# Kernel optimization log

Hardware: AMD Instinct MI355X
Metric: run time of the kernel (lower is better)

Reference implementation:

```python
import jax, jax.numpy as jnp
import numpy as np

B, H, W, C = 8, 128, 128, 384
WS, SHIFT, NH = 8, 4, 12
N = WS * WS            # tokens per window = 64
HD = C // NH           # head dim = 32
SCALE = HD ** -0.5


def _rel_pos_index():
    ch, cw = np.meshgrid(np.arange(WS), np.arange(WS), indexing='ij')
    cf = np.stack([ch.ravel(), cw.ravel()])            # (2, N)
    rel = cf[:, :, None] - cf[:, None, :]              # (2, N, N)
    rel = rel.transpose(1, 2, 0)                       # (N, N, 2)
    rel[:, :, 0] += WS - 1
    rel[:, :, 1] += WS - 1
    rel[:, :, 0] *= 2 * WS - 1
    return jnp.asarray(rel.sum(-1))                    # (N, N) int

REL_IDX = _rel_pos_index()


def _shift_mask():
    # standard Swin SW-MSA mask, built once with numpy
    img = np.zeros((1, H, W, 1), np.float32)
    cnt = 0
    for hs in (slice(0, -WS), slice(-WS, -SHIFT), slice(-SHIFT, None)):
        for ws_ in (slice(0, -WS), slice(-WS, -SHIFT), slice(-SHIFT, None)):
            img[:, hs, ws_, :] = cnt
            cnt += 1
    m = img.reshape(1, H // WS, WS, W // WS, WS, 1).transpose(0, 1, 3, 2, 4, 5)
    m = m.reshape(-1, N)                               # (nW, N)
    am = m[:, None, :] - m[:, :, None]                 # (nW, N, N)
    return np.where(am != 0, np.float32(-100.0), np.float32(0.0))


def _ln(x, g, b, eps=1e-5):
    mu = x.mean(-1, keepdims=True)
    var = ((x - mu) ** 2).mean(-1, keepdims=True)
    return (x - mu) * jax.lax.rsqrt(var + eps) * g + b


def setup_inputs() -> dict:
    key = jax.random.key(0)
    ks = jax.random.split(key, 10)
    s = 0.02
    return {
        'x': jax.random.normal(ks[0], (B, H * W, C), jnp.float32),
        'qkv_w': jax.random.normal(ks[1], (3 * C, C), jnp.float32) * s,
        'qkv_b': jnp.zeros((3 * C,), jnp.float32),
        'proj_w': jax.random.normal(ks[2], (C, C), jnp.float32) * s,
        'proj_b': jnp.zeros((C,), jnp.float32),
        'rel_bias_table': jax.random.normal(ks[3], ((2 * WS - 1) ** 2, NH), jnp.float32) * s,
        'g1': jnp.ones((C,), jnp.float32), 'b1': jnp.zeros((C,), jnp.float32),
        'g2': jnp.ones((C,), jnp.float32), 'b2': jnp.zeros((C,), jnp.float32),
        'fc1_w': jax.random.normal(ks[4], (4 * C, C), jnp.float32) * s,
        'fc1_b': jnp.zeros((4 * C,), jnp.float32),
        'fc2_w': jax.random.normal(ks[5], (C, 4 * C), jnp.float32) * s,
        'fc2_b': jnp.zeros((C,), jnp.float32),
        'attn_mask': jnp.asarray(_shift_mask()),       # (nW, N, N)
    }


def reference(x, qkv_w, qkv_b, proj_w, proj_b, rel_bias_table, g1, b1, g2, b2,
              fc1_w, fc1_b, fc2_w, fc2_b, attn_mask):
    shortcut = x
    h = _ln(x, g1, b1).reshape(B, H, W, C)
    # cyclic shift (SW-MSA)
    h = jnp.roll(h, (-SHIFT, -SHIFT), axis=(1, 2))
    # window partition -> (B*nW, N, C)
    nWh, nWw = H // WS, W // WS
    hw = h.reshape(B, nWh, WS, nWw, WS, C).transpose(0, 1, 3, 2, 4, 5)
    hw = hw.reshape(B * nWh * nWw, N, C)
    # qkv projection
    qkv = jnp.einsum('bnc,dc->bnd', hw, qkv_w) + qkv_b   # (Bw, N, 3C)
    qkv = qkv.reshape(-1, N, 3, NH, HD).transpose(2, 0, 3, 1, 4)
    q, k, v = qkv[0], qkv[1], qkv[2]                    # (Bw, NH, N, HD)
    attn = jnp.einsum('bhnd,bhmd->bhnm', q * SCALE, k)  # (Bw, NH, N, N)
    bias = rel_bias_table[REL_IDX.reshape(-1)].reshape(N, N, NH)
    attn = attn + bias.transpose(2, 0, 1)[None]
    # shift mask: attn viewed as (B, nW, NH, N, N) + mask (nW, 1, N, N)
    nW = nWh * nWw
    attn = attn.reshape(B, nW, NH, N, N) + attn_mask[None, :, None]
    attn = jax.nn.softmax(attn.reshape(-1, NH, N, N), axis=-1)
    out = jnp.einsum('bhnm,bhmd->bnhd', attn, v).reshape(-1, N, C)
    out = jnp.einsum('bnc,dc->bnd', out, proj_w) + proj_b
    # window reverse + un-shift
    out = out.reshape(B, nWh, nWw, WS, WS, C).transpose(0, 1, 3, 2, 4, 5)
    out = out.reshape(B, H, W, C)
    out = jnp.roll(out, (SHIFT, SHIFT), axis=(1, 2)).reshape(B, H * W, C)
    x = shortcut + out
    # MLP block
    h2 = _ln(x, g2, b2)
    h2 = jax.nn.gelu(jnp.einsum('blc,dc->bld', h2, fc1_w) + fc1_b, approximate=False)
    h2 = jnp.einsum('bld,cd->blc', h2, fc2_w) + fc2_b
    return x + h2
```

## Files before the change

kernel.cpp:

```cpp
#include <hip/hip_runtime.h>
#include <hip/hip_bf16.h>
#include <math.h>

typedef __attribute__((ext_vector_type(4))) float f32x4;
typedef __attribute__((ext_vector_type(8))) short bf16x8;

__device__ __forceinline__ unsigned short f2bf(float f) {
  unsigned int x = __builtin_bit_cast(unsigned int, f);
  x += 0x7fffu + ((x >> 16) & 1u);
  return (unsigned short)(x >> 16);
}
__device__ __forceinline__ float bf2f(unsigned short u) {
  unsigned int x = ((unsigned int)u) << 16;
  return __builtin_bit_cast(float, x);
}

__device__ __forceinline__ void gload_lds16(const void* g, void* l) {
  __builtin_amdgcn_global_load_lds(
      (const __attribute__((address_space(1))) unsigned int*)g,
      (__attribute__((address_space(3))) unsigned int*)l, 16, 0, 0);
}

__global__ void cvt_f32_bf16(const float* __restrict__ s, unsigned short* __restrict__ d, int n) {
  int i = blockIdx.x * 256 + threadIdx.x;
  if (i < n) d[i] = f2bf(s[i]);
}

template <int REMAP>
__global__ __launch_bounds__(256)
void ln_kernel(const float* __restrict__ x, const float* __restrict__ g,
               const float* __restrict__ b, unsigned short* __restrict__ dst_o) {
  int r = blockIdx.x * 4 + (threadIdx.x >> 6);
  int lane = threadIdx.x & 63;
  size_t src;
  if (REMAP) {
    int w = r >> 6, t = r & 63;
    int bb = w >> 8, wi = (w >> 4) & 15, wj = w & 15;
    int i = t >> 3, j = t & 7;
    int p = (wi * 8 + i + 4) & 127, q = (wj * 8 + j + 4) & 127;
    src = ((size_t)bb * 16384 + p * 128 + q) * 384;
  } else {
    src = (size_t)r * 384;
  }
  float v[6];
  float s = 0.f, s2 = 0.f;
#pragma unroll
  for (int m = 0; m < 6; ++m) {
    v[m] = x[src + lane + 64 * m];
    s += v[m];
    s2 += v[m] * v[m];
  }
#pragma unroll
  for (int o2 = 1; o2 < 64; o2 <<= 1) {
    s += __shfl_xor(s, o2);
    s2 += __shfl_xor(s2, o2);
  }
  float mu = s * (1.f / 384.f);
  float var = s2 * (1.f / 384.f) - mu * mu;
  float ri = rsqrtf(var + 1e-5f);
  size_t dst = (size_t)r * 384;
#pragma unroll
  for (int m = 0; m < 6; ++m) {
    int c = lane + 64 * m;
    dst_o[dst + c] = f2bf((v[m] - mu) * ri * g[c] + b[c]);
  }
}

__global__ __launch_bounds__(256)
void ln_bf16(const unsigned short* __restrict__ x, const float* __restrict__ g,
             const float* __restrict__ b, unsigned short* __restrict__ dst_o) {
  int r = blockIdx.x * 4 + (threadIdx.x >> 6);
  int lane = threadIdx.x & 63;
  size_t src = (size_t)r * 384;
  float v[6];
  float s = 0.f, s2 = 0.f;
#pragma unroll
  for (int m = 0; m < 3; ++m) {
    unsigned int u = *(const unsigned int*)&x[src + lane * 2 + 128 * m];
    v[2 * m] = bf2f((unsigned short)(u & 0xffffu));
    v[2 * m + 1] = bf2f((unsigned short)(u >> 16));
    s += v[2 * m] + v[2 * m + 1];
    s2 += v[2 * m] * v[2 * m] + v[2 * m + 1] * v[2 * m + 1];
  }
#pragma unroll
  for (int o2 = 1; o2 < 64; o2 <<= 1) {
    s += __shfl_xor(s, o2);
    s2 += __shfl_xor(s2, o2);
  }
  float mu = s * (1.f / 384.f);
  float var = s2 * (1.f / 384.f) - mu * mu;
  float ri = rsqrtf(var + 1e-5f);
#pragma unroll
  for (int m = 0; m < 3; ++m) {
    int c = lane * 2 + 128 * m;
    unsigned int lo = f2bf((v[2 * m] - mu) * ri * g[c] + b[c]);
    unsigned int hi = f2bf((v[2 * m + 1] - mu) * ri * g[c + 1] + b[c + 1]);
    *(unsigned int*)&dst_o[src + c] = lo | (hi << 16);
  }
}

template <int EPI>
__global__ __launch_bounds__(256, 2)
void gemm_bt(const unsigned short* __restrict__ A, const unsigned short* __restrict__ Bw,
             const float* __restrict__ bias, int M, int N, int K, int NT,
             unsigned short* __restrict__ Obf, const void* __restrict__ resid,
             float* __restrict__ Of) {
  __shared__ unsigned short smA[2][128 * 64];
  __shared__ unsigned short smB[2][128 * 64];
  const int tid = threadIdx.x;
  const int lane = tid & 63;
  const int wid = tid >> 6;
  const int wm = wid >> 1, wn = wid & 1;
  const int li = lane & 15, lg = lane >> 4;

  const int nwg = gridDim.x;
  const int orig = blockIdx.x;
  const int q = nwg >> 3, r = nwg & 7;
  const int xcd = orig & 7, loc = orig >> 3;
  const int wg = (xcd < r ? xcd * (q + 1) : r * (q + 1) + (xcd - r) * q) + loc;
  const int m0 = (wg / NT) * 128;
  const int n0 = (wg % NT) * 128;

  const int srow = wid * 8 + (lane >> 3);
  const int scol = ((lane & 7) ^ (lane >> 3)) * 8;
  const unsigned short* gA = A + (size_t)(m0 + srow) * K + scol;
  const unsigned short* gB = Bw + (size_t)(n0 + srow) * K + scol;

  f32x4 acc[4][4] = {};
  const int nk = K >> 6;
  const int fswz = (li & 7) << 3;

#pragma unroll
  for (int c = 0; c < 4; ++c) {
    gload_lds16(gA + (size_t)(c * 32) * K, &smA[0][(c * 32 + wid * 8) * 64]);
    gload_lds16(gB + (size_t)(c * 32) * K, &smB[0][(c * 32 + wid * 8) * 64]);
  }
  __syncthreads();

  for (int k0 = 0; k0 < nk; ++k0) {
    const int cur = k0 & 1;
    if (k0 + 1 < nk) {
#pragma unroll
      for (int c = 0; c < 4; ++c) {
        gload_lds16(gA + (size_t)(c * 32) * K + (k0 + 1) * 64,
                    &smA[cur ^ 1][(c * 32 + wid * 8) * 64]);
        gload_lds16(gB + (size_t)(c * 32) * K + (k0 + 1) * 64,
                    &smB[cur ^ 1][(c * 32 + wid * 8) * 64]);
      }
    }
#pragma unroll
    for (int kk = 0; kk < 2; ++kk) {
      bf16x8 a[4], bb[4];
#pragma unroll
      for (int f = 0; f < 4; ++f) {
        a[f] = *(const bf16x8*)&smA[cur][(wm * 64 + f * 16 + li) * 64 + ((kk * 32 + lg * 8) ^ fswz)];
        bb[f] = *(const bf16x8*)&smB[cur][(wn * 64 + f * 16 + li) * 64 + ((kk * 32 + lg * 8) ^ fswz)];
      }
#pragma unroll
      for (int mf = 0; mf < 4; ++mf)
#pragma unroll
        for (int nf = 0; nf < 4; ++nf)
          acc[mf][nf] = __builtin_amdgcn_mfma_f32_16x16x32_bf16(a[mf], bb[nf], acc[mf][nf], 0, 0, 0);
    }
    __syncthreads();
  }

#pragma unroll
  for (int mf = 0; mf < 4; ++mf) {
#pragma unroll
    for (int r2 = 0; r2 < 4; ++r2) {
      int mrow = m0 + wm * 64 + mf * 16 + lg * 4 + r2;
      size_t orow = (size_t)mrow;
      if (EPI == 2) {
        int w = mrow >> 6, t = mrow & 63;
        int bb2 = w >> 8, wi = (w >> 4) & 15, wj = w & 15;
        int i = t >> 3, j = t & 7;
        int p = (wi * 8 + i + 4) & 127, qq = (wj * 8 + j + 4) & 127;
        orow = (size_t)bb2 * 16384 + p * 128 + qq;
      }
#pragma unroll
      for (int nf = 0; nf < 4; ++nf) {
        int col = n0 + wn * 64 + nf * 16 + li;
        float v = acc[mf][nf][r2] + bias[col];
        if (EPI == 0) {
          Obf[(size_t)mrow * N + col] = f2bf(v);
        } else if (EPI == 1) {
          float y = 1.5957691f * (v + 0.044715f * v * v * v);
          float gl = v * __builtin_amdgcn_rcpf(1.f + __expf(-y));
          Obf[(size_t)mrow * N + col] = f2bf(gl);
        } else if (EPI == 2) {
          const float* rx = (const float*)resid;
          Obf[orow * 384 + col] = f2bf(v + rx[orow * 384 + col]);
        } else {
          const unsigned short* rx = (const unsigned short*)resid;
          Of[(size_t)mrow * N + col] = v + bf2f(rx[(size_t)mrow * N + col]);
        }
      }
    }
  }
}

__global__ __launch_bounds__(256, 2)
void attn_kernel(const unsigned short* __restrict__ qkv, const float* __restrict__ btab,
                 const float* __restrict__ mask, unsigned short* __restrict__ out) {
  __shared__ unsigned short v_lds[4][64 * 40];
  __shared__ unsigned short p_lds[4][64 * 72];
  const int w = blockIdx.x;
  const int tid = threadIdx.x;
  const int wid = tid >> 6, lane = tid & 63;
  const int li = lane & 15, lg = lane >> 4;
  const float* mrow = mask + (size_t)(w & 255) * 4096;
  const size_t base = (size_t)w * 64;
  const float SC = 0.17677669529663688f;

#pragma unroll 1
  for (int hi = 0; hi < 3; ++hi) {
    int h = wid * 3 + hi;
    bf16x8 aq[4], bk[4];
#pragma unroll
    for (int f = 0; f < 4; ++f) {
      size_t off = (base + f * 16 + li) * 1152 + h * 32 + lg * 8;
      aq[f] = *(const bf16x8*)&qkv[off];
      bk[f] = *(const bf16x8*)&qkv[off + 384];
    }
    f32x4 s[4][4] = {};
#pragma unroll
    for (int mf = 0; mf < 4; ++mf)
#pragma unroll
      for (int nf = 0; nf < 4; ++nf)
        s[mf][nf] = __builtin_amdgcn_mfma_f32_16x16x32_bf16(aq[mf], bk[nf], s[mf][nf], 0, 0, 0);

    {
      const unsigned short* vp = &qkv[(base + lane) * 1152 + 768 + h * 32];
      unsigned short* dp = &v_lds[wid][lane * 40];
#pragma unroll
      for (int c = 0; c < 4; ++c) *(bf16x8*)&dp[c * 8] = *(const bf16x8*)&vp[c * 8];
    }

#pragma unroll
    for (int mf = 0; mf < 4; ++mf) {
#pragma unroll
      for (int r = 0; r < 4; ++r) {
        int m = mf * 16 + lg * 4 + r;
        float mx = -1e30f;
#pragma unroll
        for (int nf = 0; nf < 4; ++nf) {
          int n = nf * 16 + li;
          int ridx = ((m >> 3) - (n >> 3) + 7) * 15 + (m & 7) - (n & 7) + 7;
          float val = s[mf][nf][r] * SC + btab[ridx * 12 + h] + mrow[m * 64 + n];
          s[mf][nf][r] = val;
          mx = fmaxf(mx, val);
        }
#pragma unroll
        for (int o2 = 1; o2 < 16; o2 <<= 1) mx = fmaxf(mx, __shfl_xor(mx, o2));
        float sum = 0.f;
#pragma unroll
        for (int nf = 0; nf < 4; ++nf) {
          float e = __expf(s[mf][nf][r] - mx);
          s[mf][nf][r] = e;
          sum += e;
        }
#pragma unroll
        for (int o2 = 1; o2 < 16; o2 <<= 1) sum += __shfl_xor(sum, o2);
        float inv = __builtin_amdgcn_rcpf(sum);
#pragma unroll
        for (int nf = 0; nf < 4; ++nf) s[mf][nf][r] *= inv;
      }
    }

#pragma unroll
    for (int mf = 0; mf < 4; ++mf)
#pragma unroll
      for (int nf = 0; nf < 4; ++nf)
#pragma unroll
        for (int r = 0; r < 4; ++r) {
          int m = mf * 16 + lg * 4 + r, n = nf * 16 + li;
          p_lds[wid][m * 72 + n] = f2bf(s[mf][nf][r]);
        }

    f32x4 o[4][2] = {};
#pragma unroll
    for (int kf = 0; kf < 2; ++kf) {
      bf16x8 bv[2];
#pragma unroll
      for (int df = 0; df < 2; ++df) {
        bf16x8 t;
#pragma unroll
        for (int e = 0; e < 8; ++e)
          t[e] = (short)v_lds[wid][(kf * 32 + lg * 8 + e) * 40 + df * 16 + li];
        bv[df] = t;
      }
#pragma unroll
      for (int mf = 0; mf < 4; ++mf) {
        bf16x8 pa = *(const bf16x8*)&p_lds[wid][(mf * 16 + li) * 72 + kf * 32 + lg * 8];
#pragma unroll
        for (int df = 0; df < 2; ++df)
          o[mf][df] = __builtin_amdgcn_mfma_f32_16x16x32_bf16(pa, bv[df], o[mf][df], 0, 0, 0);
      }
    }

#pragma unroll
    for (int mf = 0; mf < 4; ++mf)
#pragma unroll
      for (int df = 0; df < 2; ++df)
#pragma unroll
        for (int r = 0; r < 4; ++r) {
          size_t row = base + mf * 16 + lg * 4 + r;
          out[row * 384 + h * 32 + df * 16 + li] = f2bf(o[mf][df][r]);
        }
  }
}

extern "C" void kernel_launch(void* const* d_in, const int* in_sizes, int n_in,
                              void* d_out, int out_size, void* d_ws, size_t ws_size,
                              hipStream_t stream) {
  const float* x      = (const float*)d_in[0];
  const float* qkv_w  = (const float*)d_in[1];
  const float* qkv_b  = (const float*)d_in[2];
  const float* proj_w = (const float*)d_in[3];
  const float* proj_b = (const float*)d_in[4];
  const float* rel    = (const float*)d_in[5];
  const float* g1     = (const float*)d_in[6];
  const float* b1     = (const float*)d_in[7];
  const float* g2     = (const float*)d_in[8];
  const float* b2     = (const float*)d_in[9];
  const float* fc1_w  = (const float*)d_in[10];
  const float* fc1_b  = (const float*)d_in[11];
  const float* fc2_w  = (const float*)d_in[12];
  const float* fc2_b  = (const float*)d_in[13];
  const float* mask   = (const float*)d_in[14];
  float* out = (float*)d_out;
  char* ws = (char*)d_ws;

  const int M = 131072;
  unsigned short* hw     = (unsigned short*)ws;
  unsigned short* qkv    = (unsigned short*)(ws + 100663296);
  unsigned short* hmid   = (unsigned short*)ws;
  unsigned short* attn_o = (unsigned short*)(ws + 402653184);
  unsigned short* ln2o   = attn_o;
  unsigned short* x1b    = (unsigned short*)(ws + 503316480);
  unsigned short* wq     = (unsigned short*)(ws + 603979776);
  unsigned short* wp     = wq + 442368;
  unsigned short* w1     = wp + 147456;
  unsigned short* w2     = w1 + 589824;

  cvt_f32_bf16<<<(442368 + 255) / 256, 256, 0, stream>>>(qkv_w, wq, 442368);
  cvt_f32_bf16<<<(147456 + 255) / 256, 256, 0, stream>>>(proj_w, wp, 147456);
  cvt_f32_bf16<<<(589824 + 255) / 256, 256, 0, stream>>>(fc1_w, w1, 589824);
  cvt_f32_bf16<<<(589824 + 255) / 256, 256, 0, stream>>>(fc2_w, w2, 589824);

  ln_kernel<1><<<M / 4, 256, 0, stream>>>(x, g1, b1, hw);

  gemm_bt<0><<<9 * 1024, 256, 0, stream>>>(hw, wq, qkv_b, M, 1152, 384, 9, qkv, nullptr, nullptr);

  attn_kernel<<<2048, 256, 0, stream>>>(qkv, rel, mask, attn_o);

  gemm_bt<2><<<3 * 1024, 256, 0, stream>>>(attn_o, wp, proj_b, M, 384, 384, 3, x1b, x, nullptr);

  ln_bf16<<<M / 4, 256, 0, stream>>>(x1b, g2, b2, ln2o);

  gemm_bt<1><<<12 * 1024, 256, 0, stream>>>(ln2o, w1, fc1_b, M, 1536, 384, 12, hmid, nullptr, nullptr);

  gemm_bt<3><<<3 * 1024, 256, 0, stream>>>(hmid, w2, fc2_b, M, 384, 1536, 3, nullptr, x1b, out);
}
```

Measured before the change: 1.178 ms.

## Switch GEMMs to 256x128 tiles with 8 waves and triple-buffered LDS pipeline

Replaces the 128x128, 4-wave, double-buffered GEMM with a 256x128-tile, 512-thread kernel that uses dynamic LDS split into three stages. Loads run two K-steps ahead and are gated by explicit vmcnt waits and a raw s_barrier in place of __syncthreads. MFMA blocks are bracketed by s_setprio to favour math issue. The intent is better operand reuse and deeper latency hiding, in exchange for one workgroup per CU and 144KB of LDS, which lowers occupancy.

After: 1.145 ms. -2.8%, faster.

```diff
diff --git a/kernel.cpp b/kernel.cpp
--- a/kernel.cpp
+++ b/kernel.cpp
@@ -100,13 +100,12 @@
 }
 
 template <int EPI>
-__global__ __launch_bounds__(256, 2)
-void gemm_bt(const unsigned short* __restrict__ A, const unsigned short* __restrict__ Bw,
-             const float* __restrict__ bias, int M, int N, int K, int NT,
-             unsigned short* __restrict__ Obf, const void* __restrict__ resid,
-             float* __restrict__ Of) {
-  __shared__ unsigned short smA[2][128 * 64];
-  __shared__ unsigned short smB[2][128 * 64];
+__global__ __launch_bounds__(512, 1)
+void gemm8(const unsigned short* __restrict__ A, const unsigned short* __restrict__ Bw,
+           const float* __restrict__ bias, int M, int N, int K, int NT,
+           unsigned short* __restrict__ Obf, const void* __restrict__ resid,
+           float* __restrict__ Of) {
+  extern __shared__ unsigned short lds[];
   const int tid = threadIdx.x;
   const int lane = tid & 63;
   const int wid = tid >> 6;
@@ -118,7 +117,7 @@
   const int q = nwg >> 3, r = nwg & 7;
   const int xcd = orig & 7, loc = orig >> 3;
   const int wg = (xcd < r ? xcd * (q + 1) : r * (q + 1) + (xcd - r) * q) + loc;
-  const int m0 = (wg / NT) * 128;
+  const int m0 = (wg / NT) * 256;
   const int n0 = (wg % NT) * 128;
 
   const int srow = wid * 8 + (lane >> 3);
@@ -126,43 +125,58 @@
   const unsigned short* gA = A + (size_t)(m0 + srow) * K + scol;
   const unsigned short* gB = Bw + (size_t)(n0 + srow) * K + scol;
 
-  f32x4 acc[4][4] = {};
   const int nk = K >> 6;
   const int fswz = (li & 7) << 3;
-
-#pragma unroll
-  for (int c = 0; c < 4; ++c) {
-    gload_lds16(gA + (size_t)(c * 32) * K, &smA[0][(c * 32 + wid * 8) * 64]);
-    gload_lds16(gB + (size_t)(c * 32) * K, &smB[0][(c * 32 + wid * 8) * 64]);
-  }
-  __syncthreads();
-
-  for (int k0 = 0; k0 < nk; ++k0) {
-    const int cur = k0 & 1;
-    if (k0 + 1 < nk) {
-#pragma unroll
-      for (int c = 0; c < 4; ++c) {
-        gload_lds16(gA + (size_t)(c * 32) * K + (k0 + 1) * 64,
-                    &smA[cur ^ 1][(c * 32 + wid * 8) * 64]);
-        gload_lds16(gB + (size_t)(c * 32) * K + (k0 + 1) * 64,
-                    &smB[cur ^ 1][(c * 32 + wid * 8) * 64]);
-      }
-    }
+  f32x4 acc[4][4] = {};
+
+  auto stage = [&](int k, int b) {
+    unsigned short* dA = lds + b * 24576;
+    unsigned short* dB = dA + 16384;
+#pragma unroll
+    for (int c = 0; c < 4; ++c)
+      gload_lds16(gA + (size_t)(c * 64) * K + k * 64, &dA[c * 4096 + wid * 512]);
+#pragma unroll
+    for (int c = 0; c < 2; ++c)
+      gload_lds16(gB + (size_t)(c * 64) * K + k * 64, &dB[c * 4096 + wid * 512]);
+  };
+
+  stage(0, 0);
+  stage(1, 1);
+
+  int cur = 0;
+  for (int t = 0; t < nk; ++t) {
+    if (t < nk - 1) {
+      asm volatile("s_waitcnt vmcnt(6)" ::: "memory");
+    } else {
+      asm volatile("s_waitcnt vmcnt(0)" ::: "memory");
+    }
+    __builtin_amdgcn_s_barrier();
+    __builtin_amdgcn_sched_barrier(0);
+    if (t + 2 < nk) {
+      int nb = cur + 2;
+      if (nb >= 3) nb -= 3;
+      stage(t + 2, nb);
+    }
+    const unsigned short* pA = lds + cur * 24576;
+    const unsigned short* pB = pA + 16384;
 #pragma unroll
     for (int kk = 0; kk < 2; ++kk) {
       bf16x8 a[4], bb[4];
 #pragma unroll
       for (int f = 0; f < 4; ++f) {
-        a[f] = *(const bf16x8*)&smA[cur][(wm * 64 + f * 16 + li) * 64 + ((kk * 32 + lg * 8) ^ fswz)];
-        bb[f] = *(const bf16x8*)&smB[cur][(wn * 64 + f * 16 + li) * 64 + ((kk * 32 + lg * 8) ^ fswz)];
-      }
+        a[f] = *(const bf16x8*)&pA[(wm * 64 + f * 16 + li) * 64 + ((kk * 32 + lg * 8) ^ fswz)];
+        bb[f] = *(const bf16x8*)&pB[(wn * 64 + f * 16 + li) * 64 + ((kk * 32 + lg * 8) ^ fswz)];
+      }
+      __builtin_amdgcn_s_setprio(1);
 #pragma unroll
       for (int mf = 0; mf < 4; ++mf)
 #pragma unroll
         for (int nf = 0; nf < 4; ++nf)
           acc[mf][nf] = __builtin_amdgcn_mfma_f32_16x16x32_bf16(a[mf], bb[nf], acc[mf][nf], 0, 0, 0);
-    }
-    __syncthreads();
+      __builtin_amdgcn_s_setprio(0);
+    }
+    ++cur;
+    if (cur == 3) cur = 0;
   }
 
 #pragma unroll
@@ -333,6 +347,12 @@
   char* ws = (char*)d_ws;
 
   const int M = 131072;
+  const int LDS_BYTES = 3 * 49152;
+  (void)hipFuncSetAttribute((const void*)gemm8<0>, hipFuncAttributeMaxDynamicSharedMemorySize, LDS_BYTES);
+  (void)hipFuncSetAttribute((const void*)gemm8<1>, hipFuncAttributeMaxDynamicSharedMemorySize, LDS_BYTES);
+  (void)hipFuncSetAttribute((const void*)gemm8<2>, hipFuncAttributeMaxDynamicSharedMemorySize, LDS_BYTES);
+  (void)hipFuncSetAttribute((const void*)gemm8<3>, hipFuncAttributeMaxDynamicSharedMemorySize, LDS_BYTES);
+
   unsigned short* hw     = (unsigned short*)ws;
   unsigned short* qkv    = (unsigned short*)(ws + 100663296);
   unsigned short* hmid   = (unsigned short*)ws;
@@ -351,15 +371,15 @@
 
   ln_kernel<1><<<M / 4, 256, 0, stream>>>(x, g1, b1, hw);
 
-  gemm_bt<0><<<9 * 1024, 256, 0, stream>>>(hw, wq, qkv_b, M, 1152, 384, 9, qkv, nullptr, nullptr);
+  gemm8<0><<<512 * 9, 512, LDS_BYTES, stream>>>(hw, wq, qkv_b, M, 1152, 384, 9, qkv, nullptr, nullptr);
 
   attn_kernel<<<2048, 256, 0, stream>>>(qkv, rel, mask, attn_o);
 
-  gemm_bt<2><<<3 * 1024, 256, 0, stream>>>(attn_o, wp, proj_b, M, 384, 384, 3, x1b, x, nullptr);
+  gemm8<2><<<512 * 3, 512, LDS_BYTES, stream>>>(attn_o, wp, proj_b, M, 384, 384, 3, x1b, x, nullptr);
 
   ln_bf16<<<M / 4, 256, 0, stream>>>(x1b, g2, b2, ln2o);
 
-  gemm_bt<1><<<12 * 1024, 256, 0, stream>>>(ln2o, w1, fc1_b, M, 1536, 384, 12, hmid, nullptr, nullptr);
-
-  gemm_bt<3><<<3 * 1024, 256, 0, stream>>>(hmid, w2, fc2_b, M, 384, 1536, 3, nullptr, x1b, out);
-}
+  gemm8<1><<<512 * 12, 512, LDS_BYTES, stream>>>(ln2o, w1, fc1_b, M, 1536, 384, 12, hmid, nullptr, nullptr);
+
+  gemm8<3><<<512 * 3, 512, LDS_BYTES, stream>>>(hmid, w2, fc2_b, M, 384, 1536, 3, nullptr, x1b, out);
+}
```
